# Kernel tuning notes

Hardware: AMD Instinct MI355X
Metric: run time of the kernel (lower is better)

## Reference

```python
import jax, jax.numpy as jnp
import numpy as np

N_HEAD = 16

def setup_inputs() -> dict:
    key = jax.random.key(0)
    k1, k2, k3 = jax.random.split(key, 3)
    B, T, C = 4, 2048, 1024
    x = jax.random.normal(k1, (B, T, C), dtype=jnp.float32)
    w_qkv = jax.random.normal(k2, (C, 3 * C), dtype=jnp.float32) * (C ** -0.5)
    w_out = jax.random.normal(k3, (C, C), dtype=jnp.float32) * (C ** -0.5)
    return {"x": x, "w_qkv": w_qkv, "w_out": w_out}

def reference(x, w_qkv, w_out):
    B, T, C = x.shape
    H = N_HEAD
    d_k = C // H
    scale = d_k ** -0.5
    qkv = (x @ w_qkv).reshape(B, T, 3, H, d_k)
    q = qkv[:, :, 0].transpose(0, 2, 1, 3)  # [B,H,T,d_k]
    k = qkv[:, :, 1].transpose(0, 2, 1, 3)
    v = qkv[:, :, 2].transpose(0, 2, 1, 3)
    scores = jnp.einsum('bhqd,bhkd->bhqk', q, k) * scale  # [B,H,T,T]
    causal = jnp.tril(jnp.ones((T, T), dtype=bool))
    scores = jnp.where(causal[None, None], scores, jnp.finfo(scores.dtype).min)
    probs = jax.nn.softmax(scores, axis=-1)
    out = jnp.einsum('bhqk,bhkd->bhqd', probs, v)  # [B,H,T,d_k]
    out = out.transpose(0, 2, 1, 3).reshape(B, T, C)
    return out @ w_out
```

## Files before the change

kernel.cpp:

```cpp
#include <hip/hip_runtime.h>
#include <stdint.h>


typedef __bf16 bf16_t;
typedef __bf16 bf16x4 __attribute__((ext_vector_type(4)));
typedef __bf16 bf16x8 __attribute__((ext_vector_type(8)));
typedef float f32x4 __attribute__((ext_vector_type(4)));

#define LOG2E 1.44269504088896340736f

__device__ __forceinline__ void gl_lds16(const void* g, void* l) {
  __builtin_amdgcn_global_load_lds(
      (const __attribute__((address_space(1))) unsigned int*)g,
      (__attribute__((address_space(3))) unsigned int*)l, 16, 0, 0);
}

__device__ __forceinline__ f32x4 mfma16(bf16x8 a, bf16x8 b, f32x4 c) {
  return __builtin_amdgcn_mfma_f32_16x16x32_bf16(a, b, c, 0, 0, 0);
}

__global__ __launch_bounds__(256) void k_cvt_bf16(const float* __restrict__ in,
                                                  bf16_t* __restrict__ out, int n4) {
  int i = blockIdx.x * 256 + threadIdx.x;
  int step = gridDim.x * 256;
  for (; i < n4; i += step) {
    f32x4 v = reinterpret_cast<const f32x4*>(in)[i];
    bf16x4 o;
    o[0] = (bf16_t)v[0]; o[1] = (bf16_t)v[1];
    o[2] = (bf16_t)v[2]; o[3] = (bf16_t)v[3];
    reinterpret_cast<bf16x4*>(out)[i] = o;
  }
}

__global__ __launch_bounds__(256) void k_transpose_cvt(const float* __restrict__ in,
                                                       bf16_t* __restrict__ out,
                                                       int R, int Cc) {
  __shared__ float tile[64][65];
  const int tid = threadIdx.x;
  const int c0 = blockIdx.x * 64, r0 = blockIdx.y * 64;
  const int rr = tid >> 4, cc = (tid & 15) * 4;
#pragma unroll
  for (int i = 0; i < 4; i++) {
    f32x4 v = *reinterpret_cast<const f32x4*>(&in[(size_t)(r0 + rr + i * 16) * Cc + c0 + cc]);
    tile[rr + i * 16][cc + 0] = v[0];
    tile[rr + i * 16][cc + 1] = v[1];
    tile[rr + i * 16][cc + 2] = v[2];
    tile[rr + i * 16][cc + 3] = v[3];
  }
  __syncthreads();
  const int cr = tid >> 2, kb = (tid & 3) * 16;
#pragma unroll
  for (int j4 = 0; j4 < 4; j4++) {
    bf16x4 o;
#pragma unroll
    for (int jj = 0; jj < 4; jj++) o[jj] = (bf16_t)tile[kb + j4 * 4 + jj][cr];
    *reinterpret_cast<bf16x4*>(&out[(size_t)(c0 + cr) * R + r0 + kb + j4 * 4]) = o;
  }
}

template <int MODE>
__global__ __launch_bounds__(256) void k_gemm(const bf16_t* __restrict__ A,
                                              const bf16_t* __restrict__ Bt,
                                              void* __restrict__ C0, void* __restrict__ C1,
                                              int M, int N, int K) {
  constexpr int BM = 128, BN = 128, BK = 32;
  __shared__ bf16_t a_sh[BM * BK];
  __shared__ bf16_t b_sh[BN * BK];
  const int tid = threadIdx.x;
  const int wave = tid >> 6, lane = tid & 63;
  const int g = lane >> 4, lr = lane & 15;
  const int wm = wave >> 1, wn = wave & 1;
  const int m0 = blockIdx.y * BM, n0 = blockIdx.x * BN;
  const bf16_t* Ab = A + (size_t)m0 * K;
  const bf16_t* Bb = Bt + (size_t)n0 * K;

  f32x4 acc[4][4];
#pragma unroll
  for (int i = 0; i < 4; i++)
#pragma unroll
    for (int j = 0; j < 4; j++) acc[i][j] = (f32x4){0.f, 0.f, 0.f, 0.f};

  for (int k0 = 0; k0 < K; k0 += BK) {
#pragma unroll
    for (int i = 0; i < 2; i++) {
      int c = tid + 256 * i;
      gl_lds16(Ab + (size_t)(c >> 2) * K + k0 + (c & 3) * 8, &a_sh[c * 8]);
    }
#pragma unroll
    for (int i = 0; i < 2; i++) {
      int c = tid + 256 * i;
      gl_lds16(Bb + (size_t)(c >> 2) * K + k0 + (c & 3) * 8, &b_sh[c * 8]);
    }
    __syncthreads();
    bf16x8 af[4], bfr[4];
#pragma unroll
    for (int mi = 0; mi < 4; mi++)
      af[mi] = *reinterpret_cast<const bf16x8*>(&a_sh[(wm * 64 + mi * 16 + lr) * BK + g * 8]);
#pragma unroll
    for (int ni = 0; ni < 4; ni++)
      bfr[ni] = *reinterpret_cast<const bf16x8*>(&b_sh[(wn * 64 + ni * 16 + lr) * BK + g * 8]);
#pragma unroll
    for (int mi = 0; mi < 4; mi++)
#pragma unroll
      for (int ni = 0; ni < 4; ni++) acc[mi][ni] = mfma16(af[mi], bfr[ni], acc[mi][ni]);
    __syncthreads();
  }

#pragma unroll
  for (int mi = 0; mi < 4; mi++) {
#pragma unroll
    for (int ni = 0; ni < 4; ni++) {
      const int mb = m0 + wm * 64 + mi * 16 + g * 4;
      const int nb = n0 + wn * 64 + ni * 16;
      if constexpr (MODE == 2) {
        float* C = (float*)C0;
#pragma unroll
        for (int r = 0; r < 4; r++) C[(size_t)(mb + r) * N + nb + lr] = acc[mi][ni][r];
      } else {
        if (nb < 2048) {
          bf16_t* qk = (bf16_t*)C0;
#pragma unroll
          for (int r = 0; r < 4; r++)
            qk[(size_t)(mb + r) * 2048 + nb + lr] = (bf16_t)acc[mi][ni][r];
        } else {
          bf16_t* vT = (bf16_t*)C1;
          const int b = mb >> 11, t = mb & 2047;
          const int col = nb - 2048 + lr;
          const int h = col >> 6, d = col & 63;
          bf16x4 o;
#pragma unroll
          for (int r = 0; r < 4; r++) o[r] = (bf16_t)acc[mi][ni][r];
          *reinterpret_cast<bf16x4*>(&vT[((size_t)(b * 16 + h) * 64 + d) * 2048 + t]) = o;
        }
      }
    }
  }
}

__global__ __launch_bounds__(256) void k_attn(const bf16_t* __restrict__ qk,
                                              const bf16_t* __restrict__ vT,
                                              bf16_t* __restrict__ out) {
  constexpr int T = 2048;
  __shared__ bf16_t k_sh[2][64 * 64];
  __shared__ bf16_t v_sh[2][64 * 64];
  __shared__ bf16_t p_sh[4][32 * 72];
  const int tid = threadIdx.x;
  const int wave = tid >> 6, lane = tid & 63;
  const int g = lane >> 4, lr = lane & 15;

  const int flat = blockIdx.x;
  const int qt = 15 - (flat >> 6);
  const int s6 = flat & 63;
  const int bh = (s6 & 7) * 8 + (s6 >> 3);
  const int b = bh >> 4, h = bh & 15;
  const int q0w = qt * 128 + wave * 32;

  bf16x8 qf[2][2];
#pragma unroll
  for (int rb = 0; rb < 2; rb++) {
    const bf16_t* Qr = qk + (size_t)(b * T + q0w + rb * 16 + lr) * 2048 + h * 64;
    qf[rb][0] = *reinterpret_cast<const bf16x8*>(Qr + g * 8);
    qf[rb][1] = *reinterpret_cast<const bf16x8*>(Qr + 32 + g * 8);
  }

  f32x4 acc_o[2][4];
#pragma unroll
  for (int rb = 0; rb < 2; rb++)
#pragma unroll
    for (int dt = 0; dt < 4; dt++) acc_o[rb][dt] = (f32x4){0.f, 0.f, 0.f, 0.f};
  float mrow[2][4], lrow[2][4];
#pragma unroll
  for (int rb = 0; rb < 2; rb++)
#pragma unroll
    for (int r = 0; r < 4; r++) { mrow[rb][r] = -__builtin_inff(); lrow[rb][r] = 0.f; }

  const int nt = 2 * qt + 2;
  const bf16_t* Kbase = qk + (size_t)b * T * 2048 + 1024 + h * 64;
  const bf16_t* Vbase = vT + (size_t)bh * 64 * T;

  {
#pragma unroll
    for (int i = 0; i < 2; i++) {
      int c = tid + 256 * i;
      int row = c >> 3, col8 = (c & 7) ^ (row & 7);
      gl_lds16(Kbase + (size_t)row * 2048 + col8 * 8, &k_sh[0][c * 8]);
    }
#pragma unroll
    for (int i = 0; i < 2; i++) {
      int c = tid + 256 * i;
      int d = c >> 3, col8 = (c & 7) ^ (d & 7);
      gl_lds16(Vbase + (size_t)d * T + col8 * 8, &v_sh[0][c * 8]);
    }
  }
  __syncthreads();

  int cur = 0;
  for (int t = 0; t < nt; ++t) {
    const int kv0 = t * 64;
    if (t + 1 < nt) {
      const int kn = kv0 + 64;
#pragma unroll
      for (int i = 0; i < 2; i++) {
        int c = tid + 256 * i;
        int row = c >> 3, col8 = (c & 7) ^ (row & 7);
        gl_lds16(Kbase + (size_t)(kn + row) * 2048 + col8 * 8, &k_sh[cur ^ 1][c * 8]);
      }
#pragma unroll
      for (int i = 0; i < 2; i++) {
        int c = tid + 256 * i;
        int d = c >> 3, col8 = (c & 7) ^ (d & 7);
        gl_lds16(Vbase + (size_t)d * T + kn + col8 * 8, &v_sh[cur ^ 1][c * 8]);
      }
    }

    f32x4 s[2][4];
#pragma unroll
    for (int rb = 0; rb < 2; rb++)
#pragma unroll
      for (int kt = 0; kt < 4; kt++) s[rb][kt] = (f32x4){0.f, 0.f, 0.f, 0.f};
    __builtin_amdgcn_s_setprio(1);
#pragma unroll
    for (int kt = 0; kt < 4; kt++) {
      const int row = kt * 16 + lr, sw = row & 7;
      bf16x8 kf0 = *reinterpret_cast<const bf16x8*>(&k_sh[cur][row * 64 + (g ^ sw) * 8]);
      bf16x8 kf1 = *reinterpret_cast<const bf16x8*>(&k_sh[cur][row * 64 + ((4 + g) ^ sw) * 8]);
#pragma unroll
      for (int rb = 0; rb < 2; rb++) {
        s[rb][kt] = mfma16(qf[rb][0], kf0, s[rb][kt]);
        s[rb][kt] = mfma16(qf[rb][1], kf1, s[rb][kt]);
      }
    }
    __builtin_amdgcn_s_setprio(0);

    const float sc = 0.125f * LOG2E;
#pragma unroll
    for (int rb = 0; rb < 2; rb++)
#pragma unroll
      for (int kt = 0; kt < 4; kt++) s[rb][kt] *= sc;
    if (kv0 + 63 > q0w) {
#pragma unroll
      for (int rb = 0; rb < 2; rb++)
#pragma unroll
        for (int kt = 0; kt < 4; kt++)
#pragma unroll
          for (int r = 0; r < 4; r++)
            if (kv0 + kt * 16 + lr > q0w + rb * 16 + g * 4 + r) s[rb][kt][r] = -1e30f;
    }

#pragma unroll
    for (int rb = 0; rb < 2; rb++) {
      float rmax[4];
#pragma unroll
      for (int r = 0; r < 4; r++)
        rmax[r] = fmaxf(fmaxf(s[rb][0][r], s[rb][1][r]), fmaxf(s[rb][2][r], s[rb][3][r]));
#pragma unroll
      for (int off = 1; off < 16; off <<= 1)
#pragma unroll
        for (int r = 0; r < 4; r++) rmax[r] = fmaxf(rmax[r], __shfl_xor(rmax[r], off, 64));
      float mnew[4], alpha[4];
#pragma unroll
      for (int r = 0; r < 4; r++) {
        mnew[r] = fmaxf(mrow[rb][r], rmax[r]);
        alpha[r] = __builtin_amdgcn_exp2f(mrow[rb][r] - mnew[r]);
        mrow[rb][r] = mnew[r];
      }
      float rs[4] = {0.f, 0.f, 0.f, 0.f};
#pragma unroll
      for (int kt = 0; kt < 4; kt++) {
#pragma unroll
        for (int r = 0; r < 4; r++) {
          float p = __builtin_amdgcn_exp2f(s[rb][kt][r] - mnew[r]);
          rs[r] += p;
          p_sh[wave][(rb * 16 + g * 4 + r) * 72 + kt * 16 + lr] = (bf16_t)p;
        }
      }
#pragma unroll
      for (int off = 1; off < 16; off <<= 1)
#pragma unroll
        for (int r = 0; r < 4; r++) rs[r] += __shfl_xor(rs[r], off, 64);
#pragma unroll
      for (int r = 0; r < 4; r++) lrow[rb][r] = lrow[rb][r] * alpha[r] + rs[r];
#pragma unroll
      for (int dt = 0; dt < 4; dt++)
#pragma unroll
        for (int r = 0; r < 4; r++) acc_o[rb][dt][r] *= alpha[r];
    }

    bf16x8 pa[2][2];
#pragma unroll
    for (int rb = 0; rb < 2; rb++) {
      pa[rb][0] = *reinterpret_cast<const bf16x8*>(&p_sh[wave][(rb * 16 + lr) * 72 + g * 8]);
      pa[rb][1] = *reinterpret_cast<const bf16x8*>(&p_sh[wave][(rb * 16 + lr) * 72 + 32 + g * 8]);
    }
    __builtin_amdgcn_s_setprio(1);
#pragma unroll
    for (int dt = 0; dt < 4; dt++) {
      const int drow = dt * 16 + lr, sw = drow & 7;
      bf16x8 v0 = *reinterpret_cast<const bf16x8*>(&v_sh[cur][drow * 64 + (g ^ sw) * 8]);
      bf16x8 v1 = *reinterpret_cast<const bf16x8*>(&v_sh[cur][drow * 64 + ((4 + g) ^ sw) * 8]);
#pragma unroll
      for (int rb = 0; rb < 2; rb++) {
        acc_o[rb][dt] = mfma16(pa[rb][0], v0, acc_o[rb][dt]);
        acc_o[rb][dt] = mfma16(pa[rb][1], v1, acc_o[rb][dt]);
      }
    }
    __builtin_amdgcn_s_setprio(0);

    __syncthreads();
    cur ^= 1;
  }

#pragma unroll
  for (int rb = 0; rb < 2; rb++)
#pragma unroll
    for (int r = 0; r < 4; r++) {
      const float inv = 1.0f / lrow[rb][r];
#pragma unroll
      for (int dt = 0; dt < 4; dt++)
        out[(size_t)(b * T + q0w + rb * 16 + g * 4 + r) * 1024 + h * 64 + dt * 16 + lr] =
            (bf16_t)(acc_o[rb][dt][r] * inv);
    }
}

extern "C" void kernel_launch(void* const* d_in, const int* in_sizes, int n_in,
                              void* d_out, int out_size, void* d_ws, size_t ws_size,
                              hipStream_t stream) {
  (void)in_sizes; (void)n_in; (void)out_size; (void)ws_size;
  const float* x = (const float*)d_in[0];
  const float* w_qkv = (const float*)d_in[1];
  const float* w_out = (const float*)d_in[2];
  float* out = (float*)d_out;
  const int T = 2048, C = 1024;
  const int M = 4 * T;

  bf16_t* xb = (bf16_t*)d_ws;
  bf16_t* wqkvT = xb + (size_t)M * C;
  bf16_t* woutT = wqkvT + (size_t)3 * C * C;
  bf16_t* qkbuf = woutT + (size_t)C * C;
  bf16_t* vT = qkbuf + (size_t)M * 2 * C;
  bf16_t* attn = vT + (size_t)M * C;

  k_cvt_bf16<<<2048, 256, 0, stream>>>(x, xb, M * C / 4);
  k_transpose_cvt<<<dim3(3 * C / 64, C / 64), 256, 0, stream>>>(w_qkv, wqkvT, C, 3 * C);
  k_transpose_cvt<<<dim3(C / 64, C / 64), 256, 0, stream>>>(w_out, woutT, C, C);
  k_gemm<1><<<dim3(3 * C / 128, M / 128), 256, 0, stream>>>(xb, wqkvT, qkbuf, vT, M, 3 * C, C);
  k_attn<<<1024, 256, 0, stream>>>(qkbuf, vT, attn);
  k_gemm<2><<<dim3(C / 128, M / 128), 256, 0, stream>>>(attn, woutT, out, nullptr, M, C, C);
}
```

Measured before the change: 315.9 us.

## Double-buffer GEMM, swizzle block order, fold Q scale, lazy softmax rescale in attention

The GEMM kernel now double-buffers its A/B tiles in LDS, prefetching the next K-slice while the current one is multiplied. It also raises MFMA priority and remaps blocks into a 1D swizzled order for better L2 locality. The attention scale is folded into Q at the QKV GEMM epilogue. The attention kernel swaps MFMA operands so each lane owns a single query row, which turns the row max/sum reductions into two cross-group shuffles, and it only rescales the accumulator when the running max grows by more than 8 (log2 domain). Stores of P to LDS become vectorized. The lazy rescale threshold leaves unnormalized values up to 2^8, which trades a small precision risk for fewer exp and multiply operations.

```diff
diff --git a/kernel.cpp b/kernel.cpp
--- a/kernel.cpp
+++ b/kernel.cpp
@@ -8,6 +8,7 @@
 typedef float f32x4 __attribute__((ext_vector_type(4)));
 
 #define LOG2E 1.44269504088896340736f
+#define QSCALE (0.125f * LOG2E)
 
 __device__ __forceinline__ void gl_lds16(const void* g, void* l) {
   __builtin_amdgcn_global_load_lds(
@@ -62,15 +63,17 @@
 __global__ __launch_bounds__(256) void k_gemm(const bf16_t* __restrict__ A,
                                               const bf16_t* __restrict__ Bt,
                                               void* __restrict__ C0, void* __restrict__ C1,
-                                              int M, int N, int K) {
+                                              int M, int N, int K, int nbx) {
   constexpr int BM = 128, BN = 128, BK = 32;
-  __shared__ bf16_t a_sh[BM * BK];
-  __shared__ bf16_t b_sh[BN * BK];
+  __shared__ bf16_t a_sh[2][BM * BK];
+  __shared__ bf16_t b_sh[2][BN * BK];
   const int tid = threadIdx.x;
   const int wave = tid >> 6, lane = tid & 63;
   const int g = lane >> 4, lr = lane & 15;
   const int wm = wave >> 1, wn = wave & 1;
-  const int m0 = blockIdx.y * BM, n0 = blockIdx.x * BN;
+  const int nblk = gridDim.x;
+  const int swid = (blockIdx.x & 7) * (nblk >> 3) + (blockIdx.x >> 3);
+  const int m0 = (swid / nbx) * BM, n0 = (swid % nbx) * BN;
   const bf16_t* Ab = A + (size_t)m0 * K;
   const bf16_t* Bb = Bt + (size_t)n0 * K;
 
@@ -80,30 +83,39 @@
 #pragma unroll
     for (int j = 0; j < 4; j++) acc[i][j] = (f32x4){0.f, 0.f, 0.f, 0.f};
 
-  for (int k0 = 0; k0 < K; k0 += BK) {
+  auto stage = [&](int buf, int k0) {
 #pragma unroll
     for (int i = 0; i < 2; i++) {
       int c = tid + 256 * i;
-      gl_lds16(Ab + (size_t)(c >> 2) * K + k0 + (c & 3) * 8, &a_sh[c * 8]);
+      gl_lds16(Ab + (size_t)(c >> 2) * K + k0 + (c & 3) * 8, &a_sh[buf][c * 8]);
     }
 #pragma unroll
     for (int i = 0; i < 2; i++) {
       int c = tid + 256 * i;
-      gl_lds16(Bb + (size_t)(c >> 2) * K + k0 + (c & 3) * 8, &b_sh[c * 8]);
-    }
+      gl_lds16(Bb + (size_t)(c >> 2) * K + k0 + (c & 3) * 8, &b_sh[buf][c * 8]);
+    }
+  };
+
+  stage(0, 0);
+  __syncthreads();
+  int cur = 0;
+  for (int k0 = 0; k0 < K; k0 += BK) {
+    if (k0 + BK < K) stage(cur ^ 1, k0 + BK);
+    bf16x8 af[4], bfr[4];
+#pragma unroll
+    for (int mi = 0; mi < 4; mi++)
+      af[mi] = *reinterpret_cast<const bf16x8*>(&a_sh[cur][(wm * 64 + mi * 16 + lr) * BK + g * 8]);
+#pragma unroll
+    for (int ni = 0; ni < 4; ni++)
+      bfr[ni] = *reinterpret_cast<const bf16x8*>(&b_sh[cur][(wn * 64 + ni * 16 + lr) * BK + g * 8]);
+    __builtin_amdgcn_s_setprio(1);
+#pragma unroll
+    for (int mi = 0; mi < 4; mi++)
+#pragma unroll
+      for (int ni = 0; ni < 4; ni++) acc[mi][ni] = mfma16(af[mi], bfr[ni], acc[mi][ni]);
+    __builtin_amdgcn_s_setprio(0);
     __syncthreads();
-    bf16x8 af[4], bfr[4];
-#pragma unroll
-    for (int mi = 0; mi < 4; mi++)
-      af[mi] = *reinterpret_cast<const bf16x8*>(&a_sh[(wm * 64 + mi * 16 + lr) * BK + g * 8]);
-#pragma unroll
-    for (int ni = 0; ni < 4; ni++)
-      bfr[ni] = *reinterpret_cast<const bf16x8*>(&b_sh[(wn * 64 + ni * 16 + lr) * BK + g * 8]);
-#pragma unroll
-    for (int mi = 0; mi < 4; mi++)
-#pragma unroll
-      for (int ni = 0; ni < 4; ni++) acc[mi][ni] = mfma16(af[mi], bfr[ni], acc[mi][ni]);
-    __syncthreads();
+    cur ^= 1;
   }
 
 #pragma unroll
@@ -118,10 +130,11 @@
         for (int r = 0; r < 4; r++) C[(size_t)(mb + r) * N + nb + lr] = acc[mi][ni][r];
       } else {
         if (nb < 2048) {
+          const float scl = (nb < 1024) ? QSCALE : 1.0f;
           bf16_t* qk = (bf16_t*)C0;
 #pragma unroll
           for (int r = 0; r < 4; r++)
-            qk[(size_t)(mb + r) * 2048 + nb + lr] = (bf16_t)acc[mi][ni][r];
+            qk[(size_t)(mb + r) * 2048 + nb + lr] = (bf16_t)(acc[mi][ni][r] * scl);
         } else {
           bf16_t* vT = (bf16_t*)C1;
           const int b = mb >> 11, t = mb & 2047;
@@ -141,9 +154,10 @@
                                               const bf16_t* __restrict__ vT,
                                               bf16_t* __restrict__ out) {
   constexpr int T = 2048;
+  constexpr int PST = 72;
   __shared__ bf16_t k_sh[2][64 * 64];
   __shared__ bf16_t v_sh[2][64 * 64];
-  __shared__ bf16_t p_sh[4][32 * 72];
+  __shared__ bf16_t p_sh[4][32 * PST];
   const int tid = threadIdx.x;
   const int wave = tid >> 6, lane = tid & 63;
   const int g = lane >> 4, lr = lane & 15;
@@ -168,50 +182,35 @@
   for (int rb = 0; rb < 2; rb++)
 #pragma unroll
     for (int dt = 0; dt < 4; dt++) acc_o[rb][dt] = (f32x4){0.f, 0.f, 0.f, 0.f};
-  float mrow[2][4], lrow[2][4];
-#pragma unroll
-  for (int rb = 0; rb < 2; rb++)
-#pragma unroll
-    for (int r = 0; r < 4; r++) { mrow[rb][r] = -__builtin_inff(); lrow[rb][r] = 0.f; }
+  float mrow[2] = {-1e30f, -1e30f};
+  float lrow[2] = {0.f, 0.f};
 
   const int nt = 2 * qt + 2;
   const bf16_t* Kbase = qk + (size_t)b * T * 2048 + 1024 + h * 64;
   const bf16_t* Vbase = vT + (size_t)bh * 64 * T;
 
-  {
+  auto stageK = [&](int buf, int kv) {
 #pragma unroll
     for (int i = 0; i < 2; i++) {
       int c = tid + 256 * i;
       int row = c >> 3, col8 = (c & 7) ^ (row & 7);
-      gl_lds16(Kbase + (size_t)row * 2048 + col8 * 8, &k_sh[0][c * 8]);
+      gl_lds16(Kbase + (size_t)(kv + row) * 2048 + col8 * 8, &k_sh[buf][c * 8]);
     }
 #pragma unroll
     for (int i = 0; i < 2; i++) {
       int c = tid + 256 * i;
       int d = c >> 3, col8 = (c & 7) ^ (d & 7);
-      gl_lds16(Vbase + (size_t)d * T + col8 * 8, &v_sh[0][c * 8]);
-    }
-  }
+      gl_lds16(Vbase + (size_t)d * T + kv + col8 * 8, &v_sh[buf][c * 8]);
+    }
+  };
+
+  stageK(0, 0);
   __syncthreads();
 
   int cur = 0;
   for (int t = 0; t < nt; ++t) {
     const int kv0 = t * 64;
-    if (t + 1 < nt) {
-      const int kn = kv0 + 64;
-#pragma unroll
-      for (int i = 0; i < 2; i++) {
-        int c = tid + 256 * i;
-        int row = c >> 3, col8 = (c & 7) ^ (row & 7);
-        gl_lds16(Kbase + (size_t)(kn + row) * 2048 + col8 * 8, &k_sh[cur ^ 1][c * 8]);
-      }
-#pragma unroll
-      for (int i = 0; i < 2; i++) {
-        int c = tid + 256 * i;
-        int d = c >> 3, col8 = (c & 7) ^ (d & 7);
-        gl_lds16(Vbase + (size_t)d * T + kn + col8 * 8, &v_sh[cur ^ 1][c * 8]);
-      }
-    }
+    if (t + 1 < nt) stageK(cur ^ 1, kv0 + 64);
 
     f32x4 s[2][4];
 #pragma unroll
@@ -226,17 +225,12 @@
       bf16x8 kf1 = *reinterpret_cast<const bf16x8*>(&k_sh[cur][row * 64 + ((4 + g) ^ sw) * 8]);
 #pragma unroll
       for (int rb = 0; rb < 2; rb++) {
-        s[rb][kt] = mfma16(qf[rb][0], kf0, s[rb][kt]);
-        s[rb][kt] = mfma16(qf[rb][1], kf1, s[rb][kt]);
+        s[rb][kt] = mfma16(kf0, qf[rb][0], s[rb][kt]);
+        s[rb][kt] = mfma16(kf1, qf[rb][1], s[rb][kt]);
       }
     }
     __builtin_amdgcn_s_setprio(0);
 
-    const float sc = 0.125f * LOG2E;
-#pragma unroll
-    for (int rb = 0; rb < 2; rb++)
-#pragma unroll
-      for (int kt = 0; kt < 4; kt++) s[rb][kt] *= sc;
     if (kv0 + 63 > q0w) {
 #pragma unroll
       for (int rb = 0; rb < 2; rb++)
@@ -244,53 +238,56 @@
         for (int kt = 0; kt < 4; kt++)
 #pragma unroll
           for (int r = 0; r < 4; r++)
-            if (kv0 + kt * 16 + lr > q0w + rb * 16 + g * 4 + r) s[rb][kt][r] = -1e30f;
+            if (kv0 + kt * 16 + g * 4 + r > q0w + rb * 16 + lr) s[rb][kt][r] = -1e30f;
     }
 
 #pragma unroll
     for (int rb = 0; rb < 2; rb++) {
-      float rmax[4];
-#pragma unroll
-      for (int r = 0; r < 4; r++)
-        rmax[r] = fmaxf(fmaxf(s[rb][0][r], s[rb][1][r]), fmaxf(s[rb][2][r], s[rb][3][r]));
-#pragma unroll
-      for (int off = 1; off < 16; off <<= 1)
-#pragma unroll
-        for (int r = 0; r < 4; r++) rmax[r] = fmaxf(rmax[r], __shfl_xor(rmax[r], off, 64));
-      float mnew[4], alpha[4];
-#pragma unroll
-      for (int r = 0; r < 4; r++) {
-        mnew[r] = fmaxf(mrow[rb][r], rmax[r]);
-        alpha[r] = __builtin_amdgcn_exp2f(mrow[rb][r] - mnew[r]);
-        mrow[rb][r] = mnew[r];
-      }
-      float rs[4] = {0.f, 0.f, 0.f, 0.f};
+      float pm = s[rb][0][0];
+#pragma unroll
+      for (int kt = 0; kt < 4; kt++)
+#pragma unroll
+        for (int r = 0; r < 4; r++) pm = fmaxf(pm, s[rb][kt][r]);
+      pm = fmaxf(pm, __shfl_xor(pm, 16, 64));
+      pm = fmaxf(pm, __shfl_xor(pm, 32, 64));
+
+      unsigned long long need = __ballot(pm > mrow[rb] + 8.0f);
+      if (need) {
+        float mnew = fmaxf(mrow[rb], pm);
+        float alpha = __builtin_amdgcn_exp2f(mrow[rb] - mnew);
+        mrow[rb] = mnew;
+        lrow[rb] *= alpha;
+#pragma unroll
+        for (int r = 0; r < 4; r++) {
+          int src = (lane & 48) | ((lane >> 2) & 12) | r;
+          float ar = __shfl(alpha, src, 64);
+#pragma unroll
+          for (int dt = 0; dt < 4; dt++) acc_o[rb][dt][r] *= ar;
+        }
+      }
+
+      float rs = 0.f;
 #pragma unroll
       for (int kt = 0; kt < 4; kt++) {
-#pragma unroll
-        for (int r = 0; r < 4; r++) {
-          float p = __builtin_amdgcn_exp2f(s[rb][kt][r] - mnew[r]);
-          rs[r] += p;
-          p_sh[wave][(rb * 16 + g * 4 + r) * 72 + kt * 16 + lr] = (bf16_t)p;
-        }
-      }
-#pragma unroll
-      for (int off = 1; off < 16; off <<= 1)
-#pragma unroll
-        for (int r = 0; r < 4; r++) rs[r] += __shfl_xor(rs[r], off, 64);
-#pragma unroll
-      for (int r = 0; r < 4; r++) lrow[rb][r] = lrow[rb][r] * alpha[r] + rs[r];
-#pragma unroll
-      for (int dt = 0; dt < 4; dt++)
-#pragma unroll
-        for (int r = 0; r < 4; r++) acc_o[rb][dt][r] *= alpha[r];
+        f32x4 p;
+#pragma unroll
+        for (int r = 0; r < 4; r++) p[r] = __builtin_amdgcn_exp2f(s[rb][kt][r] - mrow[rb]);
+        rs += (p[0] + p[1]) + (p[2] + p[3]);
+        bf16x4 pb;
+#pragma unroll
+        for (int r = 0; r < 4; r++) pb[r] = (bf16_t)p[r];
+        *reinterpret_cast<bf16x4*>(&p_sh[wave][(rb * 16 + lr) * PST + kt * 16 + g * 4]) = pb;
+      }
+      rs += __shfl_xor(rs, 16, 64);
+      rs += __shfl_xor(rs, 32, 64);
+      lrow[rb] += rs;
     }
 
     bf16x8 pa[2][2];
 #pragma unroll
     for (int rb = 0; rb < 2; rb++) {
-      pa[rb][0] = *reinterpret_cast<const bf16x8*>(&p_sh[wave][(rb * 16 + lr) * 72 + g * 8]);
-      pa[rb][1] = *reinterpret_cast<const bf16x8*>(&p_sh[wave][(rb * 16 + lr) * 72 + 32 + g * 8]);
+      pa[rb][0] = *reinterpret_cast<const bf16x8*>(&p_sh[wave][(rb * 16 + lr) * PST + g * 8]);
+      pa[rb][1] = *reinterpret_cast<const bf16x8*>(&p_sh[wave][(rb * 16 + lr) * PST + 32 + g * 8]);
     }
     __builtin_amdgcn_s_setprio(1);
 #pragma unroll
@@ -311,15 +308,18 @@
   }
 
 #pragma unroll
-  for (int rb = 0; rb < 2; rb++)
+  for (int rb = 0; rb < 2; rb++) {
+    const float linv = 1.0f / lrow[rb];
 #pragma unroll
     for (int r = 0; r < 4; r++) {
-      const float inv = 1.0f / lrow[rb][r];
+      int src = (lane & 48) | ((lane >> 2) & 12) | r;
+      float lq = __shfl(linv, src, 64);
 #pragma unroll
       for (int dt = 0; dt < 4; dt++)
         out[(size_t)(b * T + q0w + rb * 16 + g * 4 + r) * 1024 + h * 64 + dt * 16 + lr] =
-            (bf16_t)(acc_o[rb][dt][r] * inv);
-    }
+            (bf16_t)(acc_o[rb][dt][r] * lq);
+    }
+  }
 }
 
 extern "C" void kernel_launch(void* const* d_in, const int* in_sizes, int n_in,
@@ -343,7 +343,9 @@
   k_cvt_bf16<<<2048, 256, 0, stream>>>(x, xb, M * C / 4);
   k_transpose_cvt<<<dim3(3 * C / 64, C / 64), 256, 0, stream>>>(w_qkv, wqkvT, C, 3 * C);
   k_transpose_cvt<<<dim3(C / 64, C / 64), 256, 0, stream>>>(w_out, woutT, C, C);
-  k_gemm<1><<<dim3(3 * C / 128, M / 128), 256, 0, stream>>>(xb, wqkvT, qkbuf, vT, M, 3 * C, C);
+  k_gemm<1><<<(3 * C / 128) * (M / 128), 256, 0, stream>>>(xb, wqkvT, qkbuf, vT, M, 3 * C, C,
+                                                           3 * C / 128);
   k_attn<<<1024, 256, 0, stream>>>(qkbuf, vT, attn);
-  k_gemm<2><<<dim3(C / 128, M / 128), 256, 0, stream>>>(attn, woutT, out, nullptr, M, C, C);
-}
+  k_gemm<2><<<(C / 128) * (M / 128), 256, 0, stream>>>(attn, woutT, out, nullptr, M, C, C,
+                                                       C / 128);
+}
```

After: 256.2 us. -18.9%, faster.
